# Kernel optimization log

Hardware: AMD Instinct MI355X
Metric: run time of the kernel (lower is better)

Reference implementation:

```python
import jax, jax.numpy as jnp
import numpy as np

B, T, D, H = 4, 4096, 1024, 64

def setup_inputs() -> dict:
    key = jax.random.key(0)
    k1, k2, k3, k4 = jax.random.split(key, 4)
    x = jax.random.normal(k1, (B, T, D), dtype=jnp.float32)
    Wk = jax.random.normal(k2, (D, H), dtype=jnp.float32) * (D ** -0.5)
    Wq = jax.random.normal(k3, (D, H), dtype=jnp.float32) * (D ** -0.5)
    Wv = jax.random.normal(k4, (D, H), dtype=jnp.float32) * (D ** -0.5)
    return {"x": x, "Wk": Wk, "Wq": Wq, "Wv": Wv}

def reference(x, Wk, Wq, Wv):
    # single-head causal self-attention (dropout inactive: training=False)
    k = x @ Wk  # [B,T,H]
    q = x @ Wq  # [B,T,H]
    v = x @ Wv  # [B,T,H]
    scale = jnp.float32(1.0) / jnp.sqrt(jnp.float32(H))
    wei = jnp.einsum('bth,bsh->bts', q, k) * scale  # [B,T,T]
    t = x.shape[1]
    causal = jnp.tril(jnp.ones((t, t), dtype=bool))[None, :, :]
    wei = jnp.where(causal, wei, jnp.float32(-jnp.inf))
    wei = jax.nn.softmax(wei, axis=-1)
    out = jnp.einsum('bts,bsh->bth', wei, v)  # [B,T,H]
    return out
```

## Files before the change

kernel.cpp:

```cpp
#include <hip/hip_runtime.h>

typedef __bf16 bf16_t;
typedef __bf16 bf16x8 __attribute__((ext_vector_type(8)));
typedef __bf16 bf16x4 __attribute__((ext_vector_type(4)));
typedef float  f32x4  __attribute__((ext_vector_type(4)));
typedef float  f32x16 __attribute__((ext_vector_type(16)));

#define B_  4
#define T_  4096
#define H_  64
#define BT  (B_*T_)

#define QSCALE 0.1803368801111204f

#define NSLOT_PB 1088
#define NSLOT    4352

#define WS_KFR  0x0000000u
#define WS_QFR  0x0200000u
#define WS_VFR  0x0400000u
#define WS_WTF  0x0600000u
#define WS_POUT 0x0680000u
#define WS_PL   0x1780000u

#define MFMA16(a,b,c) __builtin_amdgcn_mfma_f32_16x16x32_bf16((a),(b),(c),0,0,0)
#define MFMA32(a,b,c) __builtin_amdgcn_mfma_f32_32x32x16_bf16((a),(b),(c),0,0,0)

__device__ __forceinline__ unsigned pk2(float a, float b) {
  union { __bf16 h[2]; unsigned u; } u_;
  u_.h[0] = (__bf16)a; u_.h[1] = (__bf16)b;
  return u_.u;
}

__device__ __forceinline__ f32x16 zero16() {
  f32x16 z;
#pragma unroll
  for (int i = 0; i < 16; ++i) z[i] = 0.f;
  return z;
}

__global__ __launch_bounds__(128) void wtrans_kernel(
    const float* __restrict__ Wk, const float* __restrict__ Wq,
    const float* __restrict__ Wv, bf16_t* __restrict__ WTf) {
  __shared__ float lw[64][17];
  int bid = blockIdx.x;
  int nt = bid >> 4;
  int kc = bid & 15;
  int w  = nt >> 2;
  const float* W = (w == 0) ? Wk : (w == 1) ? Wq : Wv;
  float sc = (w == 1) ? QSCALE : 1.0f;
  int nl0 = (nt & 3) * 16;

  int t = threadIdx.x;
  int rr = t >> 1;
  int c0 = (t & 1) * 8;
  const float* src = W + (size_t)(kc*64 + rr)*64 + nl0 + c0;
  float4 v0 = *reinterpret_cast<const float4*>(src);
  float4 v1 = *reinterpret_cast<const float4*>(src + 4);
  lw[rr][c0+0] = v0.x; lw[rr][c0+1] = v0.y; lw[rr][c0+2] = v0.z; lw[rr][c0+3] = v0.w;
  lw[rr][c0+4] = v1.x; lw[rr][c0+5] = v1.y; lw[rr][c0+6] = v1.z; lw[rr][c0+7] = v1.w;
  __syncthreads();

  int kk   = t >> 6;
  int lane = t & 63;
  int col  = lane & 15;
  int g    = lane >> 4;
  bf16x8 o;
#pragma unroll
  for (int e = 0; e < 8; ++e) o[e] = (bf16_t)(lw[kk*32 + g*8 + e][col] * sc);
  *reinterpret_cast<bf16x8*>(WTf + ((size_t)bid*2 + kk)*512 + lane*8) = o;
}

__global__ __launch_bounds__(256) void proj_kernel(
    const float* __restrict__ x, const bf16_t* __restrict__ WTf,
    bf16_t* __restrict__ kfr, bf16_t* __restrict__ qfr, bf16_t* __restrict__ vfr) {
  __shared__ __bf16 xs[2][32][72];
  int tid  = threadIdx.x;
  int wv   = tid >> 6;
  int lane = tid & 63;
  int col  = lane & 15;
  int g    = lane >> 4;
  int m0   = blockIdx.x * 32;

  f32x4 zero4 = {0.f, 0.f, 0.f, 0.f};
  f32x4 acc[2][3];
#pragma unroll
  for (int i = 0; i < 2; ++i)
#pragma unroll
    for (int j = 0; j < 3; ++j) acc[i][j] = zero4;

  int srow = tid >> 3;
  int scol = (tid & 7) * 8;
  const float* xrow = x + (size_t)(m0 + srow)*1024 + scol;

  float4 xa[4][2];
#pragma unroll
  for (int s = 0; s < 4; ++s) {
    xa[s][0] = *reinterpret_cast<const float4*>(xrow + s*64);
    xa[s][1] = *reinterpret_cast<const float4*>(xrow + s*64 + 4);
  }
  {
    bf16x8 pk = { (bf16_t)xa[0][0].x,(bf16_t)xa[0][0].y,(bf16_t)xa[0][0].z,(bf16_t)xa[0][0].w,
                  (bf16_t)xa[0][1].x,(bf16_t)xa[0][1].y,(bf16_t)xa[0][1].z,(bf16_t)xa[0][1].w };
    *reinterpret_cast<bf16x8*>(&xs[0][srow][scol]) = pk;
  }

  const bf16_t* wtb = WTf + lane*8;
  bf16x8 bcur[6], bnxt[6];
#pragma unroll
  for (int kk = 0; kk < 2; ++kk)
#pragma unroll
    for (int nti = 0; nti < 3; ++nti)
      bcur[kk*3+nti] = *(const bf16x8*)(wtb + ((size_t)((wv*3+nti)*16 + 0)*2 + kk)*512);

#pragma unroll
  for (int t = 0; t < 16; ++t) {
    __syncthreads();
    const int cur = t & 1;
    if (t + 4 < 16) {
      xa[t & 3][0] = *reinterpret_cast<const float4*>(xrow + (t+4)*64);
      xa[t & 3][1] = *reinterpret_cast<const float4*>(xrow + (t+4)*64 + 4);
    }
    if (t + 1 < 16) {
#pragma unroll
      for (int kk = 0; kk < 2; ++kk)
#pragma unroll
        for (int nti = 0; nti < 3; ++nti)
          bnxt[kk*3+nti] = *(const bf16x8*)(wtb + ((size_t)((wv*3+nti)*16 + (t+1))*2 + kk)*512);
    }
#pragma unroll
    for (int kk = 0; kk < 2; ++kk) {
      int ko = kk*32 + g*8;
      bf16x8 f0 = *(const bf16x8*)&xs[cur][ 0 + col][ko];
      bf16x8 f1 = *(const bf16x8*)&xs[cur][16 + col][ko];
#pragma unroll
      for (int nti = 0; nti < 3; ++nti) {
        acc[0][nti] = MFMA16(f0, bcur[kk*3+nti], acc[0][nti]);
        acc[1][nti] = MFMA16(f1, bcur[kk*3+nti], acc[1][nti]);
      }
    }
    if (t + 1 < 16) {
      const int sl = (t + 1) & 3;
      bf16x8 pk = { (bf16_t)xa[sl][0].x,(bf16_t)xa[sl][0].y,(bf16_t)xa[sl][0].z,(bf16_t)xa[sl][0].w,
                    (bf16_t)xa[sl][1].x,(bf16_t)xa[sl][1].y,(bf16_t)xa[sl][1].z,(bf16_t)xa[sl][1].w };
      *reinterpret_cast<bf16x8*>(&xs[cur^1][srow][scol]) = pk;
    }
#pragma unroll
    for (int i = 0; i < 6; ++i) bcur[i] = bnxt[i];
  }
#pragma unroll
  for (int mt = 0; mt < 2; ++mt) {
    int row0 = m0 + mt*16 + 4*g;
#pragma unroll
    for (int nti = 0; nti < 3; ++nti) {
      int n = wv*48 + nti*16 + col;
      f32x4 v = acc[mt][nti];
      if (n < 128) {
        int h = n & 63;
        bf16_t* base = (n < 64) ? kfr : qfr;
#pragma unroll
        for (int r = 0; r < 4; ++r) {
          int t2 = row0 + r;
          size_t idx = (size_t)((t2>>6)*8 + ((t2>>5)&1)*4 + (h>>4))*512
                     + (size_t)((t2&31) + ((h>>3)&1)*32)*8 + (h&7);
          base[idx] = (bf16_t)v[r];
        }
      } else {
        int h = n - 128;
        size_t idx = (size_t)((row0>>6)*8 + ((h>>5)&1)*4 + ((row0>>4)&3))*512
                   + (size_t)((h&31) + ((row0>>3)&1)*32)*8 + (row0&7);
        bf16x4 pk = { (bf16_t)v[0], (bf16_t)v[1], (bf16_t)v[2], (bf16_t)v[3] };
        *reinterpret_cast<bf16x4*>(&vfr[idx]) = pk;
      }
    }
  }
}

__global__ __launch_bounds__(64) void attn_kernel(
    const bf16_t* __restrict__ qfr, const bf16_t* __restrict__ kfr,
    const bf16_t* __restrict__ vfr, bf16_t* __restrict__ pout,
    float* __restrict__ pl) {
  int l  = threadIdx.x;
  int ql = l & 31;
  int hi = l >> 5;

  int bidx = blockIdx.x;
  int b = bidx / NSLOT_PB;
  int s = bidx - b * NSLOT_PB;
  s = NSLOT_PB - 1 - s;
  int a = 0;
#pragma unroll
  for (int aa = 1; aa < 16; ++aa) if (4*aa*(aa+1) <= s) a = aa;
  int r2 = s - 4*a*(a+1);
  int qd = r2 / (a+1);
  int c  = r2 - qd*(a+1);
  int jt = 8*a + qd;
  int slot = b*NSLOT_PB + s;

  int q0    = jt << 5;
  int kv_lo = c << 8;
  int kv_hi = min(kv_lo + 256, q0 + 32);
  int ntiles = (kv_hi - kv_lo + 63) >> 6;
  int qg = q0 + ql;

  const bf16_t* qb = qfr + (size_t)((b*T_ + q0) >> 6)*4096
                   + (size_t)((q0 >> 5) & 1)*2048 + l*8;
  bf16x8 qf0 = *(const bf16x8*)(qb);
  bf16x8 qf1 = *(const bf16x8*)(qb + 512);
  bf16x8 qf2 = *(const bf16x8*)(qb + 1024);
  bf16x8 qf3 = *(const bf16x8*)(qb + 1536);

  const bf16_t* kfb = kfr + (size_t)(b*T_)*64 + l*8;
  const bf16_t* vfb = vfr + (size_t)(b*T_)*64 + l*8;

  bf16x8 kA0,kA1,kA2,kA3, kB0,kB1,kB2,kB3;
#define LOADK(kvt_) do { const bf16_t* kp_ = kfb + (size_t)(kvt_)*64;          \
    kA0=*(const bf16x8*)(kp_);        kA1=*(const bf16x8*)(kp_+512);           \
    kA2=*(const bf16x8*)(kp_+1024);   kA3=*(const bf16x8*)(kp_+1536);          \
    kB0=*(const bf16x8*)(kp_+2048);   kB1=*(const bf16x8*)(kp_+2560);          \
    kB2=*(const bf16x8*)(kp_+3072);   kB3=*(const bf16x8*)(kp_+3584); } while(0)

  LOADK(kv_lo);

  f32x16 oA = zero16(), oB = zero16();
  float l_ = 0.f;

  for (int t = 0; t < ntiles; ++t) {
    int kvt = kv_lo + t*64;
    const bf16_t* vp = vfb + (size_t)kvt*64;
    bf16x8 vA0 = *(const bf16x8*)(vp);
    bf16x8 vA1 = *(const bf16x8*)(vp + 512);
    bf16x8 vA2 = *(const bf16x8*)(vp + 1024);
    bf16x8 vA3 = *(const bf16x8*)(vp + 1536);
    bf16x8 vB0 = *(const bf16x8*)(vp + 2048);
    bf16x8 vB1 = *(const bf16x8*)(vp + 2560);
    bf16x8 vB2 = *(const bf16x8*)(vp + 3072);
    bf16x8 vB3 = *(const bf16x8*)(vp + 3584);

    f32x16 sA = zero16(), sB = zero16();
    __builtin_amdgcn_s_setprio(1);
    sA = MFMA32(kA0, qf0, sA); sB = MFMA32(kB0, qf0, sB);
    sA = MFMA32(kA1, qf1, sA); sB = MFMA32(kB1, qf1, sB);
    sA = MFMA32(kA2, qf2, sA); sB = MFMA32(kB2, qf2, sB);
    sA = MFMA32(kA3, qf3, sA); sB = MFMA32(kB3, qf3, sB);
    __builtin_amdgcn_s_setprio(0);

    if (t + 1 < ntiles) LOADK(kvt + 64);

    if (kvt + 63 > q0) {
#pragma unroll
      for (int r = 0; r < 16; ++r) {
        int kvo = kvt + (r&3) + 8*(r>>2) + 4*hi;
        if (kvo > qg)      sA[r] = -1e30f;
        if (kvo + 32 > qg) sB[r] = -1e30f;
      }
    }

    float pA[16], pB[16];
    float ts = 0.f;
#pragma unroll
    for (int r = 0; r < 16; ++r) { pA[r] = exp2f(sA[r]); ts += pA[r]; }
#pragma unroll
    for (int r = 0; r < 16; ++r) { pB[r] = exp2f(sB[r]); ts += pB[r]; }
    l_ += ts + __shfl_xor(ts, 32);

    bf16x8 p0, p1, p2, p3;
#define MKSLICES(P, F0, F1) do {                                               \
    unsigned w0 = pk2(P[0],P[1]),   w1 = pk2(P[2],P[3]);                       \
    unsigned w2 = pk2(P[4],P[5]),   w3 = pk2(P[6],P[7]);                       \
    unsigned w4 = pk2(P[8],P[9]),   w5 = pk2(P[10],P[11]);                     \
    unsigned w6 = pk2(P[12],P[13]), w7 = pk2(P[14],P[15]);                     \
    unsigned x0 = (unsigned)__shfl_xor((int)w0,32);                            \
    unsigned x1 = (unsigned)__shfl_xor((int)w1,32);                            \
    unsigned x2 = (unsigned)__shfl_xor((int)w2,32);                            \
    unsigned x3 = (unsigned)__shfl_xor((int)w3,32);                            \
    unsigned x4 = (unsigned)__shfl_xor((int)w4,32);                            \
    unsigned x5 = (unsigned)__shfl_xor((int)w5,32);                            \
    unsigned x6 = (unsigned)__shfl_xor((int)w6,32);                            \
    unsigned x7 = (unsigned)__shfl_xor((int)w7,32);                            \
    union { unsigned d[4]; bf16x8 v; } u0_, u1_;                               \
    u0_.d[0] = hi ? x2 : w0;  u0_.d[1] = hi ? x3 : w1;                         \
    u0_.d[2] = hi ? w2 : x0;  u0_.d[3] = hi ? w3 : x1;                         \
    u1_.d[0] = hi ? x6 : w4;  u1_.d[1] = hi ? x7 : w5;                         \
    u1_.d[2] = hi ? w6 : x4;  u1_.d[3] = hi ? w7 : x5;                         \
    F0 = u0_.v; F1 = u1_.v; } while(0)
    MKSLICES(pA, p0, p1);
    MKSLICES(pB, p2, p3);

    __builtin_amdgcn_s_setprio(1);
    oA = MFMA32(vA0, p0, oA); oB = MFMA32(vB0, p0, oB);
    oA = MFMA32(vA1, p1, oA); oB = MFMA32(vB1, p1, oB);
    oA = MFMA32(vA2, p2, oA); oB = MFMA32(vB2, p2, oB);
    oA = MFMA32(vA3, p3, oA); oB = MFMA32(vB3, p3, oB);
    __builtin_amdgcn_s_setprio(0);
  }

  bf16_t* po = pout + (size_t)slot * 2048;
#pragma unroll
  for (int r = 0; r < 16; ++r) {
    int h = (r&3) + 8*(r>>2) + 4*hi;
    po[h*32 + ql]      = (bf16_t)oA[r];
    po[(h+32)*32 + ql] = (bf16_t)oB[r];
  }
  if (l < 32) pl[(size_t)slot*32 + l] = l_;
}

__global__ __launch_bounds__(256) void combine_kernel(
    const bf16_t* __restrict__ pout, const float* __restrict__ pl,
    float* __restrict__ out) {
  int blk = blockIdx.x;
  int b  = blk >> 7;
  int jt = blk & 127;
  int tid = threadIdx.x;
  int wv = tid >> 6;
  int l  = tid & 63;
  int a  = jt >> 3;
  int nch = a + 1;
  int slot0 = b*NSLOT_PB + 4*a*(a+1) + (jt & 7)*(a+1);

  float oacc[8], lacc[8];
#pragma unroll
  for (int q = 0; q < 8; ++q) { oacc[q] = 0.f; lacc[q] = 0.f; }
  for (int c2 = 0; c2 < nch; ++c2) {
    const bf16_t* pp = pout + (size_t)(slot0 + c2)*2048 + l*32 + wv*8;
    bf16x8 o8 = *(const bf16x8*)pp;
    const float* plc = pl + (size_t)(slot0 + c2)*32 + wv*8;
#pragma unroll
    for (int q = 0; q < 8; ++q) { oacc[q] += (float)o8[q]; lacc[q] += plc[q]; }
  }
  float* op = out + ((size_t)b*T_ + (size_t)jt*32 + wv*8)*64 + l;
#pragma unroll
  for (int q = 0; q < 8; ++q) op[(size_t)q*64] = oacc[q] / lacc[q];
}

extern "C" void kernel_launch(void* const* d_in, const int* in_sizes, int n_in,
                              void* d_out, int out_size, void* d_ws, size_t ws_size,
                              hipStream_t stream) {
  (void)in_sizes; (void)n_in; (void)out_size; (void)ws_size;
  const float* x  = (const float*)d_in[0];
  const float* Wk = (const float*)d_in[1];
  const float* Wq = (const float*)d_in[2];
  const float* Wv = (const float*)d_in[3];
  char* ws = (char*)d_ws;
  bf16_t* kfr  = (bf16_t*)(ws + WS_KFR);
  bf16_t* qfr  = (bf16_t*)(ws + WS_QFR);
  bf16_t* vfr  = (bf16_t*)(ws + WS_VFR);
  bf16_t* WTf  = (bf16_t*)(ws + WS_WTF);
  bf16_t* pout = (bf16_t*)(ws + WS_POUT);
  float*  pl   = (float*)(ws + WS_PL);
  float*  outp = (float*)d_out;

  hipLaunchKernelGGL(wtrans_kernel,  dim3(192),   dim3(128), 0, stream, Wk, Wq, Wv, WTf);
  hipLaunchKernelGGL(proj_kernel,    dim3(512),   dim3(256), 0, stream, x, WTf, kfr, qfr, vfr);
  hipLaunchKernelGGL(attn_kernel,    dim3(NSLOT), dim3(64),  0, stream, qfr, kfr, vfr, pout, pl);
  hipLaunchKernelGGL(combine_kernel, dim3(512),   dim3(256), 0, stream, pout, pl, outp);
}
```

Measured before the change: 58.46 us.

## Stage full x tile into swizzled LDS upfront, drop per-step barriers in projection

The projection kernel now loads the entire 32x1024 x tile, converts it to bf16 and writes it into a 64KB XOR-swizzled shared buffer in one prologue with a single barrier. The K loop then runs 32 steps of MFMA with no barriers, prefetching weight fragments two steps ahead. This is meant to remove the 16 per-step __syncthreads and the double-buffered interleaving, and to avoid LDS bank conflicts. The 64KB LDS allocation limits occupancy, and the load phase no longer overlaps with compute.

Result: slower. 65.39 us (+11.9%).

```diff
diff --git a/kernel.cpp b/kernel.cpp
--- a/kernel.cpp
+++ b/kernel.cpp
@@ -74,7 +74,7 @@
 __global__ __launch_bounds__(256) void proj_kernel(
     const float* __restrict__ x, const bf16_t* __restrict__ WTf,
     bf16_t* __restrict__ kfr, bf16_t* __restrict__ qfr, bf16_t* __restrict__ vfr) {
-  __shared__ __bf16 xs[2][32][72];
+  __shared__ __align__(16) char xsb[65536];
   int tid  = threadIdx.x;
   int wv   = tid >> 6;
   int lane = tid & 63;
@@ -82,6 +82,29 @@
   int g    = lane >> 4;
   int m0   = blockIdx.x * 32;
 
+  const float* xb = x + (size_t)m0*1024 + tid*4;
+  float4 xr[2][4];
+#pragma unroll
+  for (int r = 0; r < 4; ++r) xr[0][r] = *reinterpret_cast<const float4*>(xb + r*1024);
+#pragma unroll
+  for (int bb = 0; bb < 8; ++bb) {
+    const int s = bb & 1;
+    if (bb + 1 < 8) {
+#pragma unroll
+      for (int r = 0; r < 4; ++r)
+        xr[s^1][r] = *reinterpret_cast<const float4*>(xb + ((bb+1)*4 + r)*1024);
+    }
+#pragma unroll
+    for (int r = 0; r < 4; ++r) {
+      int row = bb*4 + r;
+      float4 v = xr[s][r];
+      bf16x4 pk = { (bf16_t)v.x,(bf16_t)v.y,(bf16_t)v.z,(bf16_t)v.w };
+      int bo = row*2048 + ((tid*8) ^ ((row & 7) << 4));
+      *reinterpret_cast<bf16x4*>(xsb + bo) = pk;
+    }
+  }
+  __syncthreads();
+
   f32x4 zero4 = {0.f, 0.f, 0.f, 0.f};
   f32x4 acc[2][3];
 #pragma unroll
@@ -89,65 +112,38 @@
 #pragma unroll
     for (int j = 0; j < 3; ++j) acc[i][j] = zero4;
 
-  int srow = tid >> 3;
-  int scol = (tid & 7) * 8;
-  const float* xrow = x + (size_t)(m0 + srow)*1024 + scol;
-
-  float4 xa[4][2];
-#pragma unroll
-  for (int s = 0; s < 4; ++s) {
-    xa[s][0] = *reinterpret_cast<const float4*>(xrow + s*64);
-    xa[s][1] = *reinterpret_cast<const float4*>(xrow + s*64 + 4);
-  }
-  {
-    bf16x8 pk = { (bf16_t)xa[0][0].x,(bf16_t)xa[0][0].y,(bf16_t)xa[0][0].z,(bf16_t)xa[0][0].w,
-                  (bf16_t)xa[0][1].x,(bf16_t)xa[0][1].y,(bf16_t)xa[0][1].z,(bf16_t)xa[0][1].w };
-    *reinterpret_cast<bf16x8*>(&xs[0][srow][scol]) = pk;
-  }
-
   const bf16_t* wtb = WTf + lane*8;
-  bf16x8 bcur[6], bnxt[6];
-#pragma unroll
-  for (int kk = 0; kk < 2; ++kk)
-#pragma unroll
-    for (int nti = 0; nti < 3; ++nti)
-      bcur[kk*3+nti] = *(const bf16x8*)(wtb + ((size_t)((wv*3+nti)*16 + 0)*2 + kk)*512);
-
-#pragma unroll
-  for (int t = 0; t < 16; ++t) {
-    __syncthreads();
-    const int cur = t & 1;
-    if (t + 4 < 16) {
-      xa[t & 3][0] = *reinterpret_cast<const float4*>(xrow + (t+4)*64);
-      xa[t & 3][1] = *reinterpret_cast<const float4*>(xrow + (t+4)*64 + 4);
-    }
-    if (t + 1 < 16) {
-#pragma unroll
-      for (int kk = 0; kk < 2; ++kk)
-#pragma unroll
-        for (int nti = 0; nti < 3; ++nti)
-          bnxt[kk*3+nti] = *(const bf16x8*)(wtb + ((size_t)((wv*3+nti)*16 + (t+1))*2 + kk)*512);
-    }
-#pragma unroll
-    for (int kk = 0; kk < 2; ++kk) {
-      int ko = kk*32 + g*8;
-      bf16x8 f0 = *(const bf16x8*)&xs[cur][ 0 + col][ko];
-      bf16x8 f1 = *(const bf16x8*)&xs[cur][16 + col][ko];
-#pragma unroll
-      for (int nti = 0; nti < 3; ++nti) {
-        acc[0][nti] = MFMA16(f0, bcur[kk*3+nti], acc[0][nti]);
-        acc[1][nti] = MFMA16(f1, bcur[kk*3+nti], acc[1][nti]);
-      }
-    }
-    if (t + 1 < 16) {
-      const int sl = (t + 1) & 3;
-      bf16x8 pk = { (bf16_t)xa[sl][0].x,(bf16_t)xa[sl][0].y,(bf16_t)xa[sl][0].z,(bf16_t)xa[sl][0].w,
-                    (bf16_t)xa[sl][1].x,(bf16_t)xa[sl][1].y,(bf16_t)xa[sl][1].z,(bf16_t)xa[sl][1].w };
-      *reinterpret_cast<bf16x8*>(&xs[cur^1][srow][scol]) = pk;
-    }
-#pragma unroll
-    for (int i = 0; i < 6; ++i) bcur[i] = bnxt[i];
-  }
+  const int swz  = (col & 7) << 4;
+  const char* xr0 = xsb + col*2048;
+  const char* xr1 = xsb + (col+16)*2048;
+
+  bf16x8 bfr[2][3];
+#pragma unroll
+  for (int s = 0; s < 2; ++s)
+#pragma unroll
+    for (int n = 0; n < 3; ++n)
+      bfr[s][n] = *(const bf16x8*)(wtb + ((size_t)((wv*3+n)*32 + s))*512);
+
+#pragma unroll
+  for (int j = 0; j < 32; ++j) {
+    const int s = j & 1;
+    bf16x8 b0 = bfr[s][0], b1 = bfr[s][1], b2 = bfr[s][2];
+    if (j + 2 < 32) {
+#pragma unroll
+      for (int n = 0; n < 3; ++n)
+        bfr[s][n] = *(const bf16x8*)(wtb + ((size_t)((wv*3+n)*32 + j + 2))*512);
+    }
+    int o = (j*64 + g*16) ^ swz;
+    bf16x8 a0 = *(const bf16x8*)(xr0 + o);
+    bf16x8 a1 = *(const bf16x8*)(xr1 + o);
+    acc[0][0] = MFMA16(a0, b0, acc[0][0]);
+    acc[1][0] = MFMA16(a1, b0, acc[1][0]);
+    acc[0][1] = MFMA16(a0, b1, acc[0][1]);
+    acc[1][1] = MFMA16(a1, b1, acc[1][1]);
+    acc[0][2] = MFMA16(a0, b2, acc[0][2]);
+    acc[1][2] = MFMA16(a1, b2, acc[1][2]);
+  }
+
 #pragma unroll
   for (int mt = 0; mt < 2; ++mt) {
     int row0 = m0 + mt*16 + 4*g;
```
